# Performance work log

Hardware: AMD Instinct MI355X
Metric: run time of the kernel (lower is better)

The kernel has to match this reference:

```python
import jax, jax.numpy as jnp
import numpy as np

D_MODEL = 1024
N_HEADS = 16
HEAD_DIM = D_MODEL // N_HEADS  # 64
BUCKET = 64


def setup_inputs() -> dict:
    key = jax.random.key(0)
    k1, k2, k3 = jax.random.split(key, 3)
    B, T = 4, 4096
    x = jax.random.normal(k1, (B, T, D_MODEL), dtype=jnp.float32)
    # torch nn.Linear(d, 3d, bias=False): weight shape (3d, d), y = x @ W.T
    W_qkv = jax.random.normal(k2, (3 * D_MODEL, D_MODEL), dtype=jnp.float32) * (D_MODEL ** -0.5)
    W_out = jax.random.normal(k3, (D_MODEL, D_MODEL), dtype=jnp.float32) * (D_MODEL ** -0.5)
    return {"x": x, "W_qkv": W_qkv, "W_out": W_out}


def reference(x, W_qkv, W_out):
    B, T, _ = x.shape
    qkv = x @ W_qkv.T                                  # [B, T, 3*d_model]
    # split_heads with Hs=head_dim -> [B, 3*nH, T, Hs]; chunk along head axis
    qkv = qkv.reshape(B, T, 3 * N_HEADS, HEAD_DIM).transpose(0, 2, 1, 3)
    q, k, v = jnp.split(qkv, 3, axis=1)                # each [B, nH, T, Hs]

    q = jax.nn.softmax(q, axis=-1) * (HEAD_DIM ** -0.5)
    k = jnp.exp(k)                                     # causal path (mask is None)

    n = T // BUCKET
    bucket = lambda t: t.reshape(B, N_HEADS, n, BUCKET, HEAD_DIM)
    b_q, b_k, b_v = bucket(q), bucket(k), bucket(v)    # [B, H, n, s, d]

    # per-bucket key sums, inclusive cumsum over buckets, then shift to exclusive
    b_k_sum = jnp.sum(b_k, axis=-2)                    # [B, H, n, d]
    b_k_cumsum = jnp.cumsum(b_k_sum, axis=-2)
    b_k_cumsum = jnp.pad(b_k_cumsum, ((0, 0), (0, 0), (1, 0), (0, 0)))[:, :, :-1]

    # per-bucket kv outer products, exclusive cumsum over buckets
    context = jnp.einsum('bhnsd,bhnse->bhnde', b_k, b_v)        # [B, H, n, d, e]
    context = jnp.cumsum(context, axis=-3)
    context = jnp.pad(context, ((0, 0), (0, 0), (1, 0), (0, 0), (0, 0)))[:, :, :-1]

    den = jnp.einsum('bhnsd,bhnd->bhns', b_q, b_k_cumsum)
    D_inv = 1.0 / jnp.maximum(den, 1e-6)
    attn = jnp.einsum('bhnsd,bhnde,bhns->bhnse', b_q, context, D_inv)

    xo = attn.reshape(B, N_HEADS, T, HEAD_DIM)         # [B, H, T, Hs]
    xo = xo.transpose(0, 2, 1, 3).reshape(B, T, D_MODEL)  # cat_heads
    return xo @ W_out.T
```

## Files before the change

### kernel.cpp

```cpp
#include <hip/hip_runtime.h>
#include <hip/hip_bf16.h>
#include <math.h>

typedef __hip_bfloat16 bf16;
typedef __attribute__((ext_vector_type(4))) float f32x4;
typedef __attribute__((ext_vector_type(8))) short bf16x8s;

#define T_SEQ 4096
#define MFMA16(a, b, c) __builtin_amdgcn_mfma_f32_16x16x32_bf16(a, b, c, 0, 0, 0)
#define AS1 __attribute__((address_space(1)))
#define AS3 __attribute__((address_space(3)))

static __device__ __forceinline__ float bf2f(short u) {
    return __uint_as_float(((unsigned int)(unsigned short)u) << 16);
}
static __device__ __forceinline__ short f2bf(float f) {
    bf16 h = __float2bfloat16(f);
    union { bf16 b; short s; } c; c.b = h; return c.s;
}
static __device__ __forceinline__ int swz_f(int r) { return (r & 7) ^ (r >> 3); }

__global__ void cvt_f32_bf16(const float* __restrict__ src, bf16* __restrict__ dst, int n8) {
    int i = blockIdx.x * 256 + threadIdx.x;
    if (i >= n8) return;
    f32x4 a = ((const f32x4*)src)[(size_t)i * 2];
    f32x4 b = ((const f32x4*)src)[(size_t)i * 2 + 1];
    union { bf16 h[8]; uint4 u; } p;
    p.h[0] = __float2bfloat16(a.x); p.h[1] = __float2bfloat16(a.y);
    p.h[2] = __float2bfloat16(a.z); p.h[3] = __float2bfloat16(a.w);
    p.h[4] = __float2bfloat16(b.x); p.h[5] = __float2bfloat16(b.y);
    p.h[6] = __float2bfloat16(b.z); p.h[7] = __float2bfloat16(b.w);
    ((uint4*)dst)[i] = p.u;
}

template<int MODE>
__global__ __launch_bounds__(512, 2)
void gemm256(const bf16* __restrict__ A, const bf16* __restrict__ Bm,
             int K, int N,
             bf16* __restrict__ out0, bf16* __restrict__ ctxb, float* __restrict__ ksum,
             float* __restrict__ outf)
{
    __shared__ __align__(16) short SMEM[65536];
    const int tid  = threadIdx.x;
    const int l    = tid & 63;
    const int wid  = tid >> 6;
    const int wr   = wid >> 2;
    const int wc   = wid & 3;

    const int nwg  = gridDim.x * gridDim.y;
    const int flat = blockIdx.y * gridDim.x + blockIdx.x;
    const int swzb = (flat & 7) * (nwg >> 3) + (flat >> 3);
    const int bx   = swzb % gridDim.x;
    const int by   = swzb / gridDim.x;
    const int brow = by * 256;
    const int bcol = bx * 256;
    const int nkt  = K >> 6;

    const bool isKV = (MODE == 0) && (bx >= 4);
    const int  jkv  = bx - 4;
    const int  b0row = isKV ? (1024 + jkv * 128) : bcol;
    const int  b1row = isKV ? (2048 + jkv * 128) : bcol + 128;

    const int chnk = (l >> 4) ^ (((l & 15) >> 1) & 3);
    const short* baseA = &SMEM[(wr * 128 + (l & 15)) * 32 + chnk * 8];
    const short* baseB = &SMEM[32768 + (wc * 64 + (l & 15)) * 32 + chnk * 8];
#define RDA(BUF, KH, M_) (*(const bf16x8s*)(baseA + (BUF) * 16384 + (KH) * 8192 + (M_) * 512))
#define RDB(BUF, KH, N_) (*(const bf16x8s*)(baseB + (BUF) * 16384 + (KH) * 8192 + (N_) * 512))

    const int srow = tid >> 2;
    const int scs  = (tid & 3) ^ ((srow >> 1) & 3);
    const bf16* gA0 = A  + (size_t)(brow + srow) * K + scs * 8;
    const bf16* gA1 = A  + (size_t)(brow + 128 + srow) * K + scs * 8;
    const bf16* gB0 = Bm + (size_t)(b0row + srow) * K + scs * 8;
    const bf16* gB1 = Bm + (size_t)(b1row + srow) * K + scs * 8;
#define GLL(PTR, KH, BUF, ISB, EXTRA)                                             \
    __builtin_amdgcn_global_load_lds((const AS1 void*)((PTR) + (KH) * 32),        \
        (AS3 void*)&SMEM[(ISB) * 32768 + ((BUF) * 2 + (KH)) * 8192 + (EXTRA) + tid * 8], 16, 0, 0)

    f32x4 acc[8][4];
#pragma unroll
    for (int m = 0; m < 8; ++m)
#pragma unroll
        for (int n = 0; n < 4; ++n) acc[m][n] = (f32x4){0.f, 0.f, 0.f, 0.f};

    GLL(gA0, 0, 0, 0, 0);    GLL(gA1, 0, 0, 0, 4096);
    GLL(gB0, 0, 0, 1, 0);    GLL(gB1, 0, 0, 1, 4096);
    GLL(gA0, 1, 0, 0, 0);    GLL(gA1, 1, 0, 0, 4096);
    GLL(gB0, 1, 0, 1, 0);    GLL(gB1, 1, 0, 1, 4096);
    asm volatile("s_waitcnt vmcnt(4)" ::: "memory");
    __builtin_amdgcn_s_barrier();

    const bf16 *pA0 = gA0 + 64, *pA1 = gA1 + 64, *pB0 = gB0 + 64, *pB1 = gB1 + 64;

#define MFMA_BLOCK(ACCOFF)                                                        \
    __builtin_amdgcn_s_barrier();                                                 \
    asm volatile("s_waitcnt lgkmcnt(0)" ::: "memory");                            \
    __builtin_amdgcn_sched_barrier(0);                                            \
    __builtin_amdgcn_s_setprio(1);                                                \
    _Pragma("unroll")                                                             \
    for (int m = 0; m < 4; ++m)                                                   \
        _Pragma("unroll")                                                         \
        for (int n = 0; n < 4; ++n)                                               \
            acc[m + (ACCOFF)][n] = MFMA16(afr[m], bfr[n], acc[m + (ACCOFF)][n]);  \
    __builtin_amdgcn_s_setprio(0);                                                \
    __builtin_amdgcn_s_barrier();

#define BODY(CUR, NXT, TT)                                                        \
    {                                                                             \
        const bool pf = ((TT) + 1 < nkt);                                         \
        bf16x8s afr[4], bfr[4];                                                   \
        _Pragma("unroll") for (int n = 0; n < 4; ++n) bfr[n] = RDB(CUR, 0, n);    \
        _Pragma("unroll") for (int m = 0; m < 4; ++m) afr[m] = RDA(CUR, 0, m);    \
        if (pf) { GLL(pA0, 0, NXT, 0, 0); GLL(pA1, 0, NXT, 0, 4096); }            \
        MFMA_BLOCK(0)                                                             \
        _Pragma("unroll") for (int m = 0; m < 4; ++m) afr[m] = RDA(CUR, 0, m + 4);\
        if (pf) { GLL(pB0, 0, NXT, 1, 0); GLL(pB1, 0, NXT, 1, 4096); }            \
        asm volatile("s_waitcnt vmcnt(4)" ::: "memory");                          \
        MFMA_BLOCK(4)                                                             \
        _Pragma("unroll") for (int n = 0; n < 4; ++n) bfr[n] = RDB(CUR, 1, n);    \
        _Pragma("unroll") for (int m = 0; m < 4; ++m) afr[m] = RDA(CUR, 1, m);    \
        if (pf) { GLL(pA0, 1, NXT, 0, 0); GLL(pA1, 1, NXT, 0, 4096); }            \
        MFMA_BLOCK(0)                                                             \
        _Pragma("unroll") for (int m = 0; m < 4; ++m) afr[m] = RDA(CUR, 1, m + 4);\
        if (pf) { GLL(pB0, 1, NXT, 1, 0); GLL(pB1, 1, NXT, 1, 4096); }            \
        asm volatile("s_waitcnt vmcnt(4)" ::: "memory");                          \
        MFMA_BLOCK(4)                                                             \
        pA0 += 64; pA1 += 64; pB0 += 64; pB1 += 64;                               \
    }

    for (int t = 0; t < nkt; t += 2) {
        BODY(0, 1, t)
        BODY(1, 0, t + 1)
    }

    if (MODE == 1) {
#pragma unroll
        for (int m = 0; m < 8; ++m) {
            int row = brow + wr * 128 + m * 16 + ((l >> 4) << 2);
#pragma unroll
            for (int n = 0; n < 4; ++n) {
                int col = bcol + wc * 64 + n * 16 + (l & 15);
#pragma unroll
                for (int r = 0; r < 4; ++r)
                    outf[(size_t)(row + r) * N + col] = acc[m][n][r];
            }
        }
    } else if (!isKV) {
#pragma unroll
        for (int m = 0; m < 8; ++m) {
            int row = brow + wr * 128 + m * 16 + ((l >> 4) << 2);
#pragma unroll
            for (int r = 0; r < 4; ++r) {
                float v0 = acc[m][0][r], v1 = acc[m][1][r], v2 = acc[m][2][r], v3 = acc[m][3][r];
                float mx = fmaxf(fmaxf(v0, v1), fmaxf(v2, v3));
#pragma unroll
                for (int off = 8; off; off >>= 1) mx = fmaxf(mx, __shfl_xor(mx, off));
                float e0 = __expf(v0 - mx), e1 = __expf(v1 - mx);
                float e2 = __expf(v2 - mx), e3 = __expf(v3 - mx);
                float sm = e0 + e1 + e2 + e3;
#pragma unroll
                for (int off = 8; off; off >>= 1) sm += __shfl_xor(sm, off);
                float inv = 0.125f / sm;
                size_t rr = (size_t)(row + r);
                int cb = bcol + wc * 64 + (l & 15);
                out0[rr * 1024 + cb]      = __float2bfloat16(e0 * inv);
                out0[rr * 1024 + cb + 16] = __float2bfloat16(e1 * inv);
                out0[rr * 1024 + cb + 32] = __float2bfloat16(e2 * inv);
                out0[rr * 1024 + cb + 48] = __float2bfloat16(e3 * inv);
            }
        }
    } else {
        const int hl = wc & 1;
        short* side = (short*)SMEM + ((wc >= 2) ? 32768 : 0);
#pragma unroll
        for (int m = 0; m < 8; ++m) {
            const int ubase = wr * 16384 + (m >> 2) * 8192 + hl * 4096;
#pragma unroll
            for (int n = 0; n < 4; ++n) {
                int d = n * 16 + (l & 15);
#pragma unroll
                for (int r = 0; r < 4; ++r) {
                    int s = (m & 3) * 16 + ((l >> 4) << 2) + r;
                    float v = acc[m][n][r];
                    if (wc < 2) v = __expf(v);
                    side[ubase + d * 64 + ((((s >> 3)) ^ swz_f(d)) << 3) + (s & 7)] = f2bf(v);
                }
            }
        }
        __syncthreads();

        const int bl = wid >> 1, hu = wid & 1;
        const int gr0 = brow + bl * 64;
        const int bb  = gr0 >> 12;
        const int nb  = (gr0 & 4095) >> 6;
        const int hh  = jkv * 2 + hu;
        const size_t bid = (size_t)(bb * 16 + hh) * 64 + nb;
        const short* k_u = (const short*)SMEM + wid * 4096;
        const short* v_u = (const short*)SMEM + 32768 + wid * 4096;

        {
            float s = 0.f;
#pragma unroll
            for (int c = 0; c < 8; ++c) {
                bf16x8s kk = *(const bf16x8s*)&k_u[l * 64 + ((c ^ swz_f(l)) << 3)];
#pragma unroll
                for (int u = 0; u < 8; ++u) s += bf2f(((short*)&kk)[u]);
            }
            ksum[bid * 64 + l] = s;
        }

        f32x4 a16[4][4];
#pragma unroll
        for (int m = 0; m < 4; ++m)
#pragma unroll
            for (int n = 0; n < 4; ++n) a16[m][n] = (f32x4){0.f, 0.f, 0.f, 0.f};
#pragma unroll
        for (int kk = 0; kk < 2; ++kk) {
            const int cc = kk * 4 + (l >> 4);
            bf16x8s af[4], bf[4];
#pragma unroll
            for (int m = 0; m < 4; ++m) {
                int rA = m * 16 + (l & 15);
                af[m] = *(const bf16x8s*)&k_u[rA * 64 + ((cc ^ swz_f(rA)) << 3)];
                bf[m] = *(const bf16x8s*)&v_u[rA * 64 + ((cc ^ swz_f(rA)) << 3)];
            }
#pragma unroll
            for (int m = 0; m < 4; ++m)
#pragma unroll
                for (int n = 0; n < 4; ++n)
                    a16[m][n] = MFMA16(af[m], bf[n], a16[m][n]);
        }
        bf16* rec = ctxb + bid * 4096;
#pragma unroll
        for (int m = 0; m < 4; ++m) {
            int d0 = m * 16 + ((l >> 4) << 2);
#pragma unroll
            for (int n = 0; n < 4; ++n) {
                int e = n * 16 + (l & 15);
                ushort4 o;
                o.x = (ushort)f2bf(a16[m][n][0]); o.y = (ushort)f2bf(a16[m][n][1]);
                o.z = (ushort)f2bf(a16[m][n][2]); o.w = (ushort)f2bf(a16[m][n][3]);
                *(ushort4*)&rec[e * 64 + d0] = o;
            }
        }
    }
#undef RDA
#undef RDB
#undef GLL
#undef MFMA_BLOCK
#undef BODY
}

__global__ void cumsum_excl(const bf16* __restrict__ ctxb, const float* __restrict__ ksum,
                            bf16* __restrict__ ctp, float* __restrict__ ksump)
{
    const int bh = blockIdx.y;
    if (blockIdx.x == 4) {
        int d = threadIdx.x;
        if (d >= 64) return;
        float run = 0.f;
        for (int j = 0; j < 64; ++j) {
            size_t idx = (size_t)(bh * 64 + j) * 64 + d;
            float v = ksum[idx];
            ksump[idx] = run;
            run += v;
        }
        return;
    }
    int e0 = (blockIdx.x * 256 + threadIdx.x) * 4;
    float r0 = 0.f, r1 = 0.f, r2 = 0.f, r3 = 0.f;
    for (int j = 0; j < 64; ++j) {
        size_t idx = (size_t)(bh * 64 + j) * 4096 + e0;
        ushort4 v = *(const ushort4*)&ctxb[idx];
        ushort4 o;
        o.x = (ushort)f2bf(r0); o.y = (ushort)f2bf(r1);
        o.z = (ushort)f2bf(r2); o.w = (ushort)f2bf(r3);
        *(ushort4*)&ctp[idx] = o;
        r0 += bf2f((short)v.x); r1 += bf2f((short)v.y);
        r2 += bf2f((short)v.z); r3 += bf2f((short)v.w);
    }
}

__global__ __launch_bounds__(256)
void bucket_attn(const bf16* __restrict__ Qb, const bf16* __restrict__ ctp,
                 const float* __restrict__ ksump, bf16* __restrict__ attn)
{
    __shared__ __align__(16) short q_bf[64 * 64];
    __shared__ __align__(16) short ct_bf[64 * 64];
    __shared__ __align__(16) short at_s[64 * 72];
    __shared__ float dinv_s[64];
    __shared__ float ksum_s[64];
    const int bid = blockIdx.x;
    const int bh = bid >> 6, n = bid & 63;
    const int b = bh >> 4, h = bh & 15;
    const size_t rowbase = (size_t)(b * T_SEQ + n * 64) * 1024 + h * 64;
    const int tid = threadIdx.x;
    const int l = tid & 63, w = tid >> 6;

#pragma unroll
    for (int j = 0; j < 2; ++j) {
        int i = tid + 256 * j;
        int e = i >> 3, dc = i & 7;
        bf16x8s cv = *(const bf16x8s*)&ctp[(size_t)bid * 4096 + e * 64 + dc * 8];
        *(bf16x8s*)&ct_bf[e * 64 + ((dc ^ swz_f(e)) << 3)] = cv;
    }
    if (tid < 64) ksum_s[tid] = ksump[(size_t)bid * 64 + tid];
    __syncthreads();

#pragma unroll
    for (int i = 0; i < 16; ++i) {
        int s = w * 16 + i;
        float qv = bf2f(*(const short*)&Qb[rowbase + (size_t)s * 1024 + l]);
        float dp = qv * ksum_s[l];
#pragma unroll
        for (int off = 32; off; off >>= 1) dp += __shfl_xor(dp, off);
        if (l == 0) dinv_s[s] = 1.f / fmaxf(dp, 1e-6f);
        q_bf[s * 64 + ((((l >> 3)) ^ swz_f(s)) << 3) + (l & 7)] = f2bf(qv);
    }
    __syncthreads();

    f32x4 acc[4];
#pragma unroll
    for (int i = 0; i < 4; ++i) acc[i] = (f32x4){0.f, 0.f, 0.f, 0.f};
    bf16x8s afr[2], bfr[2][4];
#pragma unroll
    for (int kk = 0; kk < 2; ++kk) {
        int cc = kk * 4 + (l >> 4);
        int r = w * 16 + (l & 15);
        afr[kk] = *(const bf16x8s*)&q_bf[r * 64 + ((cc ^ swz_f(r)) << 3)];
#pragma unroll
        for (int n4 = 0; n4 < 4; ++n4) {
            int e = n4 * 16 + (l & 15);
            bfr[kk][n4] = *(const bf16x8s*)&ct_bf[e * 64 + ((cc ^ swz_f(e)) << 3)];
        }
    }
#pragma unroll
    for (int kk = 0; kk < 2; ++kk)
#pragma unroll
        for (int n4 = 0; n4 < 4; ++n4)
            acc[n4] = MFMA16(afr[kk], bfr[kk][n4], acc[n4]);

#pragma unroll
    for (int n4 = 0; n4 < 4; ++n4) {
        int e = n4 * 16 + (l & 15);
#pragma unroll
        for (int r = 0; r < 4; ++r) {
            int s = w * 16 + ((l >> 4) << 2) + r;
            at_s[s * 72 + e] = f2bf(acc[n4][r] * dinv_s[s]);
        }
    }
    __syncthreads();

#pragma unroll
    for (int j = 0; j < 2; ++j) {
        int i = tid + 256 * j;
        int s = i >> 3, c = i & 7;
        bf16x8s v = *(const bf16x8s*)&at_s[s * 72 + c * 8];
        *(bf16x8s*)&attn[rowbase + (size_t)s * 1024 + c * 8] = v;
    }
}

extern "C" void kernel_launch(void* const* d_in, const int* in_sizes, int n_in,
                              void* d_out, int out_size, void* d_ws, size_t ws_size,
                              hipStream_t stream)
{
    const float* x    = (const float*)d_in[0];
    const float* Wqkv = (const float*)d_in[1];
    const float* Wout = (const float*)d_in[2];

    char* ws = (char*)d_ws;
    size_t off = 0;
    auto alloc = [&](size_t bytes) { void* p = ws + off; off += (bytes + 255) & ~(size_t)255; return p; };
    bf16*  xb    = (bf16*)alloc((size_t)16384 * 1024 * 2);
    bf16*  wqkvb = (bf16*)alloc((size_t)3072 * 1024 * 2);
    bf16*  woutb = (bf16*)alloc((size_t)1024 * 1024 * 2);
    bf16*  Qb    = (bf16*)alloc((size_t)16384 * 1024 * 2);
    bf16*  ctxb  = (bf16*)alloc((size_t)4096 * 4096 * 2);
    float* ksum  = (float*)alloc((size_t)4096 * 64 * 4);
    bf16*  ctp   = (bf16*)alloc((size_t)4096 * 4096 * 2);
    float* ksump = (float*)alloc((size_t)4096 * 64 * 4);
    bf16*  attnb = xb;
    float* outf  = (float*)d_out;

    cvt_f32_bf16<<<dim3(16384 * 1024 / 8 / 256), 256, 0, stream>>>(x, xb, 16384 * 1024 / 8);
    cvt_f32_bf16<<<dim3(3072 * 1024 / 8 / 256), 256, 0, stream>>>(Wqkv, wqkvb, 3072 * 1024 / 8);
    cvt_f32_bf16<<<dim3(1024 * 1024 / 8 / 256), 256, 0, stream>>>(Wout, woutb, 1024 * 1024 / 8);

    gemm256<0><<<dim3(12, 64), 512, 0, stream>>>(xb, wqkvb, 1024, 3072, Qb, ctxb, ksum, nullptr);
    cumsum_excl<<<dim3(5, 64), 256, 0, stream>>>(ctxb, ksum, ctp, ksump);
    bucket_attn<<<dim3(4096), 256, 0, stream>>>(Qb, ctp, ksump, attnb);
    gemm256<1><<<dim3(4, 64), 512, 0, stream>>>(attnb, woutb, 1024, 1024, nullptr, nullptr, nullptr, outf);
}
```

Measured before the change: 231.9 us.

## Fuse context cumsum into attention kernel via chunked two-level scan

Replaces the full exclusive cumsum, which wrote a complete prefix-context buffer, with a coarse scan that stores only the prefix at every 8th bucket. The attention kernel now walks 8 consecutive buckets per block, keeping a running fp32 prefix in shared memory and adding each bucket's context as it goes. This removes the large ctp write and read traffic. The key-sum is now computed from the exp values in registers inside the QKV GEMM epilogue, instead of being re-read from LDS. The cost is far fewer attention blocks (512 instead of 4096) running a serial 8-step loop, so there is less parallelism and latency hiding.

```diff
diff --git a/kernel.cpp b/kernel.cpp
--- a/kernel.cpp
+++ b/kernel.cpp
@@ -172,42 +172,57 @@
     } else {
         const int hl = wc & 1;
         short* side = (short*)SMEM + ((wc >= 2) ? 32768 : 0);
+        float ks[2][4];
+#pragma unroll
+        for (int u = 0; u < 2; ++u)
+#pragma unroll
+            for (int n = 0; n < 4; ++n) ks[u][n] = 0.f;
 #pragma unroll
         for (int m = 0; m < 8; ++m) {
             const int ubase = wr * 16384 + (m >> 2) * 8192 + hl * 4096;
+            const int s0 = (m & 3) * 16 + ((l >> 4) << 2);
+            const int sc = s0 >> 3, slo = s0 & 7;
 #pragma unroll
             for (int n = 0; n < 4; ++n) {
                 int d = n * 16 + (l & 15);
-#pragma unroll
-                for (int r = 0; r < 4; ++r) {
-                    int s = (m & 3) * 16 + ((l >> 4) << 2) + r;
-                    float v = acc[m][n][r];
-                    if (wc < 2) v = __expf(v);
-                    side[ubase + d * 64 + ((((s >> 3)) ^ swz_f(d)) << 3) + (s & 7)] = f2bf(v);
+                union { short h4[4]; uint2 u2; } pk;
+                if (wc < 2) {
+                    float e0 = __expf(acc[m][n][0]), e1 = __expf(acc[m][n][1]);
+                    float e2 = __expf(acc[m][n][2]), e3 = __expf(acc[m][n][3]);
+                    ks[m >> 2][n] += (e0 + e1) + (e2 + e3);
+                    pk.h4[0] = f2bf(e0); pk.h4[1] = f2bf(e1);
+                    pk.h4[2] = f2bf(e2); pk.h4[3] = f2bf(e3);
+                } else {
+                    pk.h4[0] = f2bf(acc[m][n][0]); pk.h4[1] = f2bf(acc[m][n][1]);
+                    pk.h4[2] = f2bf(acc[m][n][2]); pk.h4[3] = f2bf(acc[m][n][3]);
                 }
-            }
+                *(uint2*)&side[ubase + d * 64 + ((sc ^ swz_f(d)) << 3) + slo] = pk.u2;
+            }
+        }
+        if (wc < 2) {
+#pragma unroll
+            for (int u = 0; u < 2; ++u)
+#pragma unroll
+                for (int n = 0; n < 4; ++n) {
+                    float s = ks[u][n];
+                    s += __shfl_xor(s, 16);
+                    s += __shfl_xor(s, 32);
+                    if ((l >> 4) == 0) {
+                        int unit = wr * 4 + u * 2 + hl;
+                        int gr0 = brow + (unit >> 1) * 64;
+                        size_t bidu = (size_t)(((gr0 >> 12) * 16) + jkv * 2 + (unit & 1)) * 64
+                                      + ((gr0 & 4095) >> 6);
+                        ksum[bidu * 64 + n * 16 + (l & 15)] = s;
+                    }
+                }
         }
         __syncthreads();
 
-        const int bl = wid >> 1, hu = wid & 1;
-        const int gr0 = brow + bl * 64;
-        const int bb  = gr0 >> 12;
-        const int nb  = (gr0 & 4095) >> 6;
-        const int hh  = jkv * 2 + hu;
-        const size_t bid = (size_t)(bb * 16 + hh) * 64 + nb;
+        const int gr0 = brow + (wid >> 1) * 64;
+        const size_t bid = (size_t)(((gr0 >> 12) * 16) + jkv * 2 + (wid & 1)) * 64
+                           + ((gr0 & 4095) >> 6);
         const short* k_u = (const short*)SMEM + wid * 4096;
         const short* v_u = (const short*)SMEM + 32768 + wid * 4096;
-
-        {
-            float s = 0.f;
-#pragma unroll
-            for (int c = 0; c < 8; ++c) {
-                bf16x8s kk = *(const bf16x8s*)&k_u[l * 64 + ((c ^ swz_f(l)) << 3)];
-#pragma unroll
-                for (int u = 0; u < 8; ++u) s += bf2f(((short*)&kk)[u]);
-            }
-            ksum[bid * 64 + l] = s;
-        }
 
         f32x4 a16[4][4];
 #pragma unroll
@@ -251,112 +266,126 @@
 #undef BODY
 }
 
-__global__ void cumsum_excl(const bf16* __restrict__ ctxb, const float* __restrict__ ksum,
-                            bf16* __restrict__ ctp, float* __restrict__ ksump)
+__global__ void scan8(const bf16* __restrict__ ctxb, const float* __restrict__ ksum,
+                      float* __restrict__ C16, float* __restrict__ Ks16)
 {
     const int bh = blockIdx.y;
     if (blockIdx.x == 4) {
         int d = threadIdx.x;
         if (d >= 64) return;
         float run = 0.f;
-        for (int j = 0; j < 64; ++j) {
-            size_t idx = (size_t)(bh * 64 + j) * 64 + d;
-            float v = ksum[idx];
-            ksump[idx] = run;
-            run += v;
+        Ks16[(size_t)(bh * 8) * 64 + d] = 0.f;
+        for (int j = 0; j < 56; ++j) {
+            run += ksum[(size_t)(bh * 64 + j) * 64 + d];
+            if ((j & 7) == 7) Ks16[(size_t)(bh * 8 + (j >> 3) + 1) * 64 + d] = run;
         }
         return;
     }
-    int e0 = (blockIdx.x * 256 + threadIdx.x) * 4;
-    float r0 = 0.f, r1 = 0.f, r2 = 0.f, r3 = 0.f;
-    for (int j = 0; j < 64; ++j) {
-        size_t idx = (size_t)(bh * 64 + j) * 4096 + e0;
-        ushort4 v = *(const ushort4*)&ctxb[idx];
-        ushort4 o;
-        o.x = (ushort)f2bf(r0); o.y = (ushort)f2bf(r1);
-        o.z = (ushort)f2bf(r2); o.w = (ushort)f2bf(r3);
-        *(ushort4*)&ctp[idx] = o;
-        r0 += bf2f((short)v.x); r1 += bf2f((short)v.y);
-        r2 += bf2f((short)v.z); r3 += bf2f((short)v.w);
-    }
-}
-
-__global__ __launch_bounds__(256)
-void bucket_attn(const bf16* __restrict__ Qb, const bf16* __restrict__ ctp,
-                 const float* __restrict__ ksump, bf16* __restrict__ attn)
+    int e0 = blockIdx.x * 1024 + threadIdx.x * 4;
+    f32x4 run = {0.f, 0.f, 0.f, 0.f};
+    *(f32x4*)&C16[(size_t)(bh * 8) * 4096 + e0] = run;
+    for (int j = 0; j < 56; ++j) {
+        ushort4 v = *(const ushort4*)&ctxb[(size_t)(bh * 64 + j) * 4096 + e0];
+        run.x += bf2f((short)v.x); run.y += bf2f((short)v.y);
+        run.z += bf2f((short)v.z); run.w += bf2f((short)v.w);
+        if ((j & 7) == 7) *(f32x4*)&C16[(size_t)(bh * 8 + (j >> 3) + 1) * 4096 + e0] = run;
+    }
+}
+
+__global__ __launch_bounds__(512)
+void attn_scan(const bf16* __restrict__ Qb, const bf16* __restrict__ ctxb,
+               const float* __restrict__ ksum, const float* __restrict__ C16,
+               const float* __restrict__ Ks16, bf16* __restrict__ attn)
 {
-    __shared__ __align__(16) short q_bf[64 * 64];
-    __shared__ __align__(16) short ct_bf[64 * 64];
+    __shared__ __align__(16) float Pf[4096];
+    __shared__ __align__(16) short ctb[4096];
+    __shared__ __align__(16) short qb[4096];
     __shared__ __align__(16) short at_s[64 * 72];
-    __shared__ float dinv_s[64];
-    __shared__ float ksum_s[64];
-    const int bid = blockIdx.x;
-    const int bh = bid >> 6, n = bid & 63;
+    __shared__ float kp[64];
+    __shared__ float dinv[64];
+    const int ck = blockIdx.x, bh = blockIdx.y;
+    const int tid = threadIdx.x, l = tid & 63, w = tid >> 6;
+
+    const size_t base16 = (size_t)(bh * 8 + ck) * 4096;
+    *(f32x4*)&Pf[tid * 8]     = *(const f32x4*)&C16[base16 + tid * 8];
+    *(f32x4*)&Pf[tid * 8 + 4] = *(const f32x4*)&C16[base16 + tid * 8 + 4];
+    if (tid < 64) kp[tid] = Ks16[(size_t)(bh * 8 + ck) * 64 + tid];
+    __syncthreads();
+
     const int b = bh >> 4, h = bh & 15;
-    const size_t rowbase = (size_t)(b * T_SEQ + n * 64) * 1024 + h * 64;
-    const int tid = threadIdx.x;
-    const int l = tid & 63, w = tid >> 6;
-
-#pragma unroll
-    for (int j = 0; j < 2; ++j) {
-        int i = tid + 256 * j;
-        int e = i >> 3, dc = i & 7;
-        bf16x8s cv = *(const bf16x8s*)&ctp[(size_t)bid * 4096 + e * 64 + dc * 8];
-        *(bf16x8s*)&ct_bf[e * 64 + ((dc ^ swz_f(e)) << 3)] = cv;
-    }
-    if (tid < 64) ksum_s[tid] = ksump[(size_t)bid * 64 + tid];
-    __syncthreads();
-
-#pragma unroll
-    for (int i = 0; i < 16; ++i) {
-        int s = w * 16 + i;
-        float qv = bf2f(*(const short*)&Qb[rowbase + (size_t)s * 1024 + l]);
-        float dp = qv * ksum_s[l];
-#pragma unroll
-        for (int off = 32; off; off >>= 1) dp += __shfl_xor(dp, off);
-        if (l == 0) dinv_s[s] = 1.f / fmaxf(dp, 1e-6f);
-        q_bf[s * 64 + ((((l >> 3)) ^ swz_f(s)) << 3) + (l & 7)] = f2bf(qv);
-    }
-    __syncthreads();
-
-    f32x4 acc[4];
-#pragma unroll
-    for (int i = 0; i < 4; ++i) acc[i] = (f32x4){0.f, 0.f, 0.f, 0.f};
-    bf16x8s afr[2], bfr[2][4];
-#pragma unroll
-    for (int kk = 0; kk < 2; ++kk) {
-        int cc = kk * 4 + (l >> 4);
-        int r = w * 16 + (l & 15);
-        afr[kk] = *(const bf16x8s*)&q_bf[r * 64 + ((cc ^ swz_f(r)) << 3)];
-#pragma unroll
-        for (int n4 = 0; n4 < 4; ++n4) {
-            int e = n4 * 16 + (l & 15);
-            bfr[kk][n4] = *(const bf16x8s*)&ct_bf[e * 64 + ((cc ^ swz_f(e)) << 3)];
-        }
-    }
-#pragma unroll
-    for (int kk = 0; kk < 2; ++kk)
-#pragma unroll
-        for (int n4 = 0; n4 < 4; ++n4)
-            acc[n4] = MFMA16(afr[kk], bfr[kk][n4], acc[n4]);
-
-#pragma unroll
-    for (int n4 = 0; n4 < 4; ++n4) {
-        int e = n4 * 16 + (l & 15);
-#pragma unroll
-        for (int r = 0; r < 4; ++r) {
-            int s = w * 16 + ((l >> 4) << 2) + r;
-            at_s[s * 72 + e] = f2bf(acc[n4][r] * dinv_s[s]);
-        }
-    }
-    __syncthreads();
-
-#pragma unroll
-    for (int j = 0; j < 2; ++j) {
-        int i = tid + 256 * j;
-        int s = i >> 3, c = i & 7;
-        bf16x8s v = *(const bf16x8s*)&at_s[s * 72 + c * 8];
-        *(bf16x8s*)&attn[rowbase + (size_t)s * 1024 + c * 8] = v;
+    const int e_r = tid >> 3, dc_r = tid & 7;
+    const int ctbaddr = e_r * 64 + ((dc_r ^ swz_f(e_r)) << 3);
+    const int sg = w & 3, eh = w >> 2;
+
+#pragma unroll 1
+    for (int jj = 0; jj < 8; ++jj) {
+        const int j = ck * 8 + jj;
+        const size_t rowbase = ((size_t)(b * T_SEQ + j * 64)) * 1024 + h * 64;
+        {
+            f32x4 lo = *(const f32x4*)&Pf[tid * 8];
+            f32x4 hi = *(const f32x4*)&Pf[tid * 8 + 4];
+            union { short h8[8]; uint4 u; } pk;
+            pk.h8[0] = f2bf(lo.x); pk.h8[1] = f2bf(lo.y);
+            pk.h8[2] = f2bf(lo.z); pk.h8[3] = f2bf(lo.w);
+            pk.h8[4] = f2bf(hi.x); pk.h8[5] = f2bf(hi.y);
+            pk.h8[6] = f2bf(hi.z); pk.h8[7] = f2bf(hi.w);
+            *(uint4*)&ctb[ctbaddr] = pk.u;
+        }
+#pragma unroll
+        for (int i = 0; i < 8; ++i) {
+            int s = w * 8 + i;
+            float qv = bf2f(*(const short*)&Qb[rowbase + (size_t)s * 1024 + l]);
+            float dp = qv * kp[l];
+#pragma unroll
+            for (int off = 32; off; off >>= 1) dp += __shfl_xor(dp, off);
+            if (l == 0) dinv[s] = 1.f / fmaxf(dp, 1e-6f);
+            qb[s * 64 + (((l >> 3) ^ swz_f(s)) << 3) + (l & 7)] = f2bf(qv);
+        }
+        __syncthreads();
+        f32x4 acc2[2];
+        acc2[0] = (f32x4){0.f, 0.f, 0.f, 0.f};
+        acc2[1] = (f32x4){0.f, 0.f, 0.f, 0.f};
+#pragma unroll
+        for (int kk = 0; kk < 2; ++kk) {
+            int cc = kk * 4 + (l >> 4);
+            int sA = sg * 16 + (l & 15);
+            bf16x8s af = *(const bf16x8s*)&qb[sA * 64 + ((cc ^ swz_f(sA)) << 3)];
+#pragma unroll
+            for (int n = 0; n < 2; ++n) {
+                int e = eh * 32 + n * 16 + (l & 15);
+                bf16x8s bf_ = *(const bf16x8s*)&ctb[e * 64 + ((cc ^ swz_f(e)) << 3)];
+                acc2[n] = MFMA16(af, bf_, acc2[n]);
+            }
+        }
+        {
+            const size_t cb = (size_t)(bh * 64 + j) * 4096 + tid * 8;
+            ushort4 v0 = *(const ushort4*)&ctxb[cb];
+            ushort4 v1 = *(const ushort4*)&ctxb[cb + 4];
+            f32x4 lo = *(const f32x4*)&Pf[tid * 8];
+            f32x4 hi = *(const f32x4*)&Pf[tid * 8 + 4];
+            lo.x += bf2f((short)v0.x); lo.y += bf2f((short)v0.y);
+            lo.z += bf2f((short)v0.z); lo.w += bf2f((short)v0.w);
+            hi.x += bf2f((short)v1.x); hi.y += bf2f((short)v1.y);
+            hi.z += bf2f((short)v1.z); hi.w += bf2f((short)v1.w);
+            *(f32x4*)&Pf[tid * 8]     = lo;
+            *(f32x4*)&Pf[tid * 8 + 4] = hi;
+        }
+        if (tid < 64) kp[tid] += ksum[(size_t)(bh * 64 + j) * 64 + tid];
+#pragma unroll
+        for (int n = 0; n < 2; ++n) {
+            int e = eh * 32 + n * 16 + (l & 15);
+#pragma unroll
+            for (int r = 0; r < 4; ++r) {
+                int s = sg * 16 + ((l >> 4) << 2) + r;
+                at_s[s * 72 + e] = f2bf(acc2[n][r] * dinv[s]);
+            }
+        }
+        __syncthreads();
+        {
+            int s = tid >> 3, c = tid & 7;
+            bf16x8s vv = *(const bf16x8s*)&at_s[s * 72 + c * 8];
+            *(bf16x8s*)&attn[rowbase + (size_t)s * 1024 + c * 8] = vv;
+        }
     }
 }
 
@@ -377,8 +406,8 @@
     bf16*  Qb    = (bf16*)alloc((size_t)16384 * 1024 * 2);
     bf16*  ctxb  = (bf16*)alloc((size_t)4096 * 4096 * 2);
     float* ksum  = (float*)alloc((size_t)4096 * 64 * 4);
-    bf16*  ctp   = (bf16*)alloc((size_t)4096 * 4096 * 2);
-    float* ksump = (float*)alloc((size_t)4096 * 64 * 4);
+    float* C16   = (float*)alloc((size_t)64 * 8 * 4096 * 4);
+    float* Ks16  = (float*)alloc((size_t)64 * 8 * 64 * 4);
     bf16*  attnb = xb;
     float* outf  = (float*)d_out;
 
@@ -387,7 +416,7 @@
     cvt_f32_bf16<<<dim3(1024 * 1024 / 8 / 256), 256, 0, stream>>>(Wout, woutb, 1024 * 1024 / 8);
 
     gemm256<0><<<dim3(12, 64), 512, 0, stream>>>(xb, wqkvb, 1024, 3072, Qb, ctxb, ksum, nullptr);
-    cumsum_excl<<<dim3(5, 64), 256, 0, stream>>>(ctxb, ksum, ctp, ksump);
-    bucket_attn<<<dim3(4096), 256, 0, stream>>>(Qb, ctp, ksump, attnb);
+    scan8<<<dim3(5, 64), 256, 0, stream>>>(ctxb, ksum, C16, Ks16);
+    attn_scan<<<dim3(8, 64), 512, 0, stream>>>(Qb, ctxb, ksum, C16, Ks16, attnb);
     gemm256<1><<<dim3(4, 64), 512, 0, stream>>>(attnb, woutb, 1024, 1024, nullptr, nullptr, nullptr, outf);
 }
```

Result: no change. 232.3 us (+0.2%).

## Restructure GEMM main loop into two phases and fuse key sums into epilogue

Applied to the files above, without the earlier changes.

The GEMM k-loop drops from four barrier-separated MFMA blocks per tile to two phases. Each phase waits on its global-to-LDS loads once, reads all eight A fragments, issues every prefetch for the next stage, and then runs 32 MFMAs. This removes barriers and waits, at the cost of more registers held for the A fragments. The QKV epilogue now writes packed 4-element bf16 stores and computes the per-bucket key sums in registers with shuffles, replacing a second pass over LDS. Those sums are taken in fp32 before rounding to bf16, so they differ slightly from the old values.

```diff
diff --git a/kernel.cpp b/kernel.cpp
--- a/kernel.cpp
+++ b/kernel.cpp
@@ -87,44 +87,35 @@
     GLL(gB0, 0, 0, 1, 0);    GLL(gB1, 0, 0, 1, 4096);
     GLL(gA0, 1, 0, 0, 0);    GLL(gA1, 1, 0, 0, 4096);
     GLL(gB0, 1, 0, 1, 0);    GLL(gB1, 1, 0, 1, 4096);
-    asm volatile("s_waitcnt vmcnt(4)" ::: "memory");
-    __builtin_amdgcn_s_barrier();
 
     const bf16 *pA0 = gA0 + 64, *pA1 = gA1 + 64, *pB0 = gB0 + 64, *pB1 = gB1 + 64;
 
-#define MFMA_BLOCK(ACCOFF)                                                        \
-    __builtin_amdgcn_s_barrier();                                                 \
-    asm volatile("s_waitcnt lgkmcnt(0)" ::: "memory");                            \
-    __builtin_amdgcn_sched_barrier(0);                                            \
-    __builtin_amdgcn_s_setprio(1);                                                \
-    _Pragma("unroll")                                                             \
-    for (int m = 0; m < 4; ++m)                                                   \
+#define PHASE(CUR, NXT, KS, PF)                                                   \
+    {                                                                             \
+        bf16x8s afr[8], bfr[4];                                                   \
+        if (PF) { asm volatile("s_waitcnt vmcnt(4)" ::: "memory"); }              \
+        else    { asm volatile("s_waitcnt vmcnt(0)" ::: "memory"); }              \
+        __builtin_amdgcn_s_barrier();                                             \
+        __builtin_amdgcn_sched_barrier(0);                                        \
+        _Pragma("unroll") for (int n = 0; n < 4; ++n) bfr[n] = RDB(CUR, KS, n);   \
+        _Pragma("unroll") for (int m = 0; m < 8; ++m) afr[m] = RDA(CUR, KS, m);   \
+        if (PF) { GLL(pA0, KS, NXT, 0, 0); GLL(pA1, KS, NXT, 0, 4096);            \
+                  GLL(pB0, KS, NXT, 1, 0); GLL(pB1, KS, NXT, 1, 4096); }          \
+        __builtin_amdgcn_s_setprio(1);                                            \
         _Pragma("unroll")                                                         \
-        for (int n = 0; n < 4; ++n)                                               \
-            acc[m + (ACCOFF)][n] = MFMA16(afr[m], bfr[n], acc[m + (ACCOFF)][n]);  \
-    __builtin_amdgcn_s_setprio(0);                                                \
-    __builtin_amdgcn_s_barrier();
+        for (int m = 0; m < 8; ++m)                                               \
+            _Pragma("unroll")                                                     \
+            for (int n = 0; n < 4; ++n)                                           \
+                acc[m][n] = MFMA16(afr[m], bfr[n], acc[m][n]);                    \
+        __builtin_amdgcn_s_setprio(0);                                            \
+        __builtin_amdgcn_s_barrier();                                             \
+    }
 
 #define BODY(CUR, NXT, TT)                                                        \
     {                                                                             \
         const bool pf = ((TT) + 1 < nkt);                                         \
-        bf16x8s afr[4], bfr[4];                                                   \
-        _Pragma("unroll") for (int n = 0; n < 4; ++n) bfr[n] = RDB(CUR, 0, n);    \
-        _Pragma("unroll") for (int m = 0; m < 4; ++m) afr[m] = RDA(CUR, 0, m);    \
-        if (pf) { GLL(pA0, 0, NXT, 0, 0); GLL(pA1, 0, NXT, 0, 4096); }            \
-        MFMA_BLOCK(0)                                                             \
-        _Pragma("unroll") for (int m = 0; m < 4; ++m) afr[m] = RDA(CUR, 0, m + 4);\
-        if (pf) { GLL(pB0, 0, NXT, 1, 0); GLL(pB1, 0, NXT, 1, 4096); }            \
-        asm volatile("s_waitcnt vmcnt(4)" ::: "memory");                          \
-        MFMA_BLOCK(4)                                                             \
-        _Pragma("unroll") for (int n = 0; n < 4; ++n) bfr[n] = RDB(CUR, 1, n);    \
-        _Pragma("unroll") for (int m = 0; m < 4; ++m) afr[m] = RDA(CUR, 1, m);    \
-        if (pf) { GLL(pA0, 1, NXT, 0, 0); GLL(pA1, 1, NXT, 0, 4096); }            \
-        MFMA_BLOCK(0)                                                             \
-        _Pragma("unroll") for (int m = 0; m < 4; ++m) afr[m] = RDA(CUR, 1, m + 4);\
-        if (pf) { GLL(pB0, 1, NXT, 1, 0); GLL(pB1, 1, NXT, 1, 4096); }            \
-        asm volatile("s_waitcnt vmcnt(4)" ::: "memory");                          \
-        MFMA_BLOCK(4)                                                             \
+        PHASE(CUR, NXT, 0, pf)                                                    \
+        PHASE(CUR, NXT, 1, pf)                                                    \
         pA0 += 64; pA1 += 64; pB0 += 64; pB1 += 64;                               \
     }
 
@@ -172,42 +163,57 @@
     } else {
         const int hl = wc & 1;
         short* side = (short*)SMEM + ((wc >= 2) ? 32768 : 0);
+        float ks[2][4];
+#pragma unroll
+        for (int u = 0; u < 2; ++u)
+#pragma unroll
+            for (int n = 0; n < 4; ++n) ks[u][n] = 0.f;
 #pragma unroll
         for (int m = 0; m < 8; ++m) {
             const int ubase = wr * 16384 + (m >> 2) * 8192 + hl * 4096;
+            const int s0 = (m & 3) * 16 + ((l >> 4) << 2);
+            const int sc = s0 >> 3, slo = s0 & 7;
 #pragma unroll
             for (int n = 0; n < 4; ++n) {
                 int d = n * 16 + (l & 15);
-#pragma unroll
-                for (int r = 0; r < 4; ++r) {
-                    int s = (m & 3) * 16 + ((l >> 4) << 2) + r;
-                    float v = acc[m][n][r];
-                    if (wc < 2) v = __expf(v);
-                    side[ubase + d * 64 + ((((s >> 3)) ^ swz_f(d)) << 3) + (s & 7)] = f2bf(v);
+                union { short h4[4]; uint2 u2; } pk;
+                if (wc < 2) {
+                    float e0 = __expf(acc[m][n][0]), e1 = __expf(acc[m][n][1]);
+                    float e2 = __expf(acc[m][n][2]), e3 = __expf(acc[m][n][3]);
+                    ks[m >> 2][n] += (e0 + e1) + (e2 + e3);
+                    pk.h4[0] = f2bf(e0); pk.h4[1] = f2bf(e1);
+                    pk.h4[2] = f2bf(e2); pk.h4[3] = f2bf(e3);
+                } else {
+                    pk.h4[0] = f2bf(acc[m][n][0]); pk.h4[1] = f2bf(acc[m][n][1]);
+                    pk.h4[2] = f2bf(acc[m][n][2]); pk.h4[3] = f2bf(acc[m][n][3]);
                 }
-            }
+                *(uint2*)&side[ubase + d * 64 + ((sc ^ swz_f(d)) << 3) + slo] = pk.u2;
+            }
+        }
+        if (wc < 2) {
+#pragma unroll
+            for (int u = 0; u < 2; ++u)
+#pragma unroll
+                for (int n = 0; n < 4; ++n) {
+                    float s = ks[u][n];
+                    s += __shfl_xor(s, 16);
+                    s += __shfl_xor(s, 32);
+                    if ((l >> 4) == 0) {
+                        int unit = wr * 4 + u * 2 + hl;
+                        int gr0 = brow + (unit >> 1) * 64;
+                        size_t bidu = (size_t)(((gr0 >> 12) * 16) + jkv * 2 + (unit & 1)) * 64
+                                      + ((gr0 & 4095) >> 6);
+                        ksum[bidu * 64 + n * 16 + (l & 15)] = s;
+                    }
+                }
         }
         __syncthreads();
 
-        const int bl = wid >> 1, hu = wid & 1;
-        const int gr0 = brow + bl * 64;
-        const int bb  = gr0 >> 12;
-        const int nb  = (gr0 & 4095) >> 6;
-        const int hh  = jkv * 2 + hu;
-        const size_t bid = (size_t)(bb * 16 + hh) * 64 + nb;
+        const int gr0 = brow + (wid >> 1) * 64;
+        const size_t bid = (size_t)(((gr0 >> 12) * 16) + jkv * 2 + (wid & 1)) * 64
+                           + ((gr0 & 4095) >> 6);
         const short* k_u = (const short*)SMEM + wid * 4096;
         const short* v_u = (const short*)SMEM + 32768 + wid * 4096;
-
-        {
-            float s = 0.f;
-#pragma unroll
-            for (int c = 0; c < 8; ++c) {
-                bf16x8s kk = *(const bf16x8s*)&k_u[l * 64 + ((c ^ swz_f(l)) << 3)];
-#pragma unroll
-                for (int u = 0; u < 8; ++u) s += bf2f(((short*)&kk)[u]);
-            }
-            ksum[bid * 64 + l] = s;
-        }
 
         f32x4 a16[4][4];
 #pragma unroll
@@ -247,7 +253,7 @@
 #undef RDA
 #undef RDB
 #undef GLL
-#undef MFMA_BLOCK
+#undef PHASE
 #undef BODY
 }
 
```

Measured after the change: 239.6 us. 3.4% more time.
